# Optimization experiments

Hardware: AMD Instinct MI355X
Metric: run time of the kernel (lower is better)

Reference implementation:

```python
import jax, jax.numpy as jnp
import numpy as np

B, A, HR = 2, 180, 512
H_OUT = W_OUT = 512


def setup_inputs() -> dict:
    key = jax.random.key(0)
    k1, = jax.random.split(key, 1)
    sino = jax.random.normal(k1, (B, A, HR), dtype=jnp.float32)
    angles_deg = jnp.linspace(0.0, 180.0, A, endpoint=False, dtype=jnp.float32)
    return {"sino": sino, "angles_deg": angles_deg, "H": H_OUT, "W": W_OUT}


def _forward(sino, angles_deg, H, W):
    Bn, An, Hr = sino.shape
    pad = int(1.0 * 0.1 * min(H, W))  # pad_ratio = 1.0
    Hp, Wp = H + 2 * pad, W + 2 * pad

    # --- F.interpolate bilinear, align_corners=False: (A,B,Hr,1) -> (A,B,Hp,Wp).
    # Input width is 1, so width interp replicates the single column; only height interp matters.
    src = jnp.clip((jnp.arange(Hp, dtype=jnp.float32) + 0.5) * (Hr / Hp) - 0.5, 0.0, Hr - 1)
    i0 = jnp.floor(src).astype(jnp.int32)
    i1 = jnp.minimum(i0 + 1, Hr - 1)
    wH = src - i0.astype(jnp.float32)
    p = jnp.transpose(sino, (1, 0, 2)).astype(jnp.float32)  # (A,B,Hr)
    col = p[:, :, i0] * (1.0 - wH) + p[:, :, i1] * wH       # (A,B,Hp)
    proj = jnp.broadcast_to(col[:, :, :, None], (An, Bn, Hp, Wp))  # (A,B,Hp,Wp)

    # --- affine_grid (align_corners=False), sign = -1
    th = -jnp.deg2rad(angles_deg)
    c, s = jnp.cos(th), jnp.sin(th)                          # (A,)
    xs = (jnp.arange(Wp, dtype=jnp.float32) + 0.5) * (2.0 / Wp) - 1.0
    ys = (jnp.arange(Hp, dtype=jnp.float32) + 0.5) * (2.0 / Hp) - 1.0
    gx = c[:, None, None] * xs[None, None, :] - s[:, None, None] * ys[None, :, None]  # (A,Hp,Wp)
    gy = s[:, None, None] * xs[None, None, :] + c[:, None, None] * ys[None, :, None]

    # --- grid_sample bilinear, zeros padding, align_corners=False
    ix = ((gx + 1.0) * Wp - 1.0) * 0.5
    iy = ((gy + 1.0) * Hp - 1.0) * 0.5
    x0 = jnp.floor(ix).astype(jnp.int32); x1 = x0 + 1
    y0 = jnp.floor(iy).astype(jnp.int32); y1 = y0 + 1
    wx = ix - x0.astype(jnp.float32)
    wy = iy - y0.astype(jnp.float32)

    def corner(img, xi, yi, w):  # img (B,Hp,Wp); idx/w (Hp,Wp)
        valid = (xi >= 0) & (xi <= Wp - 1) & (yi >= 0) & (yi <= Hp - 1)
        xc = jnp.clip(xi, 0, Wp - 1)
        yc = jnp.clip(yi, 0, Hp - 1)
        return img[:, yc, xc] * (w * valid.astype(jnp.float32))[None]

    def sample(img, x0a, x1a, y0a, y1a, wxa, wya):
        return (corner(img, x0a, y0a, (1 - wxa) * (1 - wya)) +
                corner(img, x1a, y0a, wxa * (1 - wya)) +
                corner(img, x0a, y1a, (1 - wxa) * wya) +
                corner(img, x1a, y1a, wxa * wya))

    xr = jax.vmap(sample)(proj, x0, x1, y0, y1, wx, wy)      # (A,B,Hp,Wp)
    acc = xr.sum(axis=0) / (An + 1e-06)                      # (B,Hp,Wp)
    acc = acc[:, None, :, :]                                 # (B,1,Hp,Wp)
    if pad > 0:
        acc = acc[:, :, pad:Hp - pad, pad:Wp - pad]
    return acc


def reference(sino, angles_deg, H, W):
    return _forward(sino, angles_deg, H, W)
```

## Files before the change

### kernel.cpp

```cpp
#include <hip/hip_runtime.h>
#include <hip/hip_fp16.h>
#include <math.h>

#define B_N   2
#define A_N   180
#define HR_N  512
#define H_OUT 512
#define W_OUT 512
#define PAD   51
#define HP    614
#define WP    614
#define GUARD 80
#define HPP   (HP + 2*GUARD)
#define NPIX  (H_OUT * W_OUT)

#define TW    16
#define TH    8
#define QA    45
#define CH_Q  15
#define NCH   3
#define WIN   20


__device__ __forceinline__ float col_val(const float* __restrict__ sino,
                                         int b, int a, int yy) {
    if (yy < 0 || yy >= HP) return 0.0f;
    float src = ((float)yy + 0.5f) * ((float)HR_N / (float)HP) - 0.5f;
    src = fminf(fmaxf(src, 0.0f), (float)(HR_N - 1));
    int i0 = (int)floorf(src);
    int i1 = min(i0 + 1, HR_N - 1);
    float wH = src - (float)i0;
    const float* srow = sino + ((size_t)b * A_N + a) * HR_N;
    return srow[i0] * (1.0f - wH) + srow[i1] * wH;
}

__global__ void prep_kernel(const float* __restrict__ sino,
                            const float* __restrict__ angles,
                            uint2* __restrict__ pk2,
                            float2* __restrict__ tg) {
    int idx = blockIdx.x * blockDim.x + threadIdx.x;
    if (idx < A_N) {
        float th = -angles[idx] * (float)(M_PI / 180.0);
        tg[idx] = make_float2(cosf(th), sinf(th));
    }
    const int total = A_N * HPP;
    if (idx < total) {
        int y = idx % HPP;
        int a = idx / HPP;
        int yy = y - GUARD;
        float v00 = col_val(sino, 0, a, yy);
        float v10 = col_val(sino, 1, a, yy);
        float v01 = col_val(sino, 0, a, yy + 1);
        float v11 = col_val(sino, 1, a, yy + 1);
        __half2 lo = __floats2half2_rn(v00, v10);
        __half2 hi = __floats2half2_rn(v01, v11);
        uint2 u;
        u.x = *(unsigned int*)&lo;
        u.y = *(unsigned int*)&hi;
        pk2[idx] = u;
    }
}

template <bool INTERIOR>
__device__ __forceinline__ void bp_body(const uint2* __restrict__ pk2,
                                        const float4* __restrict__ s_cs,
                                        const unsigned* __restrict__ s_off,
                                        uint2* __restrict__ s_win,
                                        int t, int q, float X, float Y,
                                        float& a00, float& a01, float& a10, float& a11) {
    for (int ch = 0; ch < NCH; ++ch) {
        for (int e = t; e < 4 * CH_Q * WIN; e += 256) {
            int wid = e / WIN;
            int j   = e - wid * WIN;
            int qq  = wid / CH_Q;
            int la  = wid - qq * CH_Q;
            int a   = qq * QA + ch * CH_Q + la;
            s_win[e] = pk2[s_off[a] + (unsigned)j];
        }
        __syncthreads();

        const int abase = q * QA + ch * CH_Q;
        const int wbase = q * (CH_Q * WIN);
        if (INTERIOR) {
            __half2 h0 = __float2half2_rn(0.0f);
            __half2 h1 = __float2half2_rn(0.0f);
#pragma unroll
            for (int la = 0; la < CH_Q; ++la) {
                float4 cs = s_cs[abase + la];
                float c = cs.x, s = cs.y;
                float f0 = fmaf(s, X, fmaf(c, Y, cs.z));
                float f1 = f0 + s;
                int   li0 = (int)f0;  float wy0 = __builtin_amdgcn_fractf(f0);
                int   li1 = (int)f1;  float wy1 = f1 - (float)li1;
                uint2 cv0 = s_win[wbase + la * WIN + li0];
                uint2 cv1 = s_win[wbase + la * WIN + li1];
                __half2 lo0 = *(__half2*)&cv0.x, hi0 = *(__half2*)&cv0.y;
                __half2 lo1 = *(__half2*)&cv1.x, hi1 = *(__half2*)&cv1.y;
                h0 = __hadd2(h0, __hfma2(__float2half2_rn(wy0), __hsub2(hi0, lo0), lo0));
                h1 = __hadd2(h1, __hfma2(__float2half2_rn(wy1), __hsub2(hi1, lo1), lo1));
            }
            a00 += __low2float(h0);  a01 += __high2float(h0);
            a10 += __low2float(h1);  a11 += __high2float(h1);
        } else {
#pragma unroll
            for (int la = 0; la < CH_Q; ++la) {
                float4 cs = s_cs[abase + la];
                float c = cs.x, s = cs.y;
                float f0 = fmaf(s, X, fmaf(c, Y, cs.z));
                float f1 = f0 + s;
                int   li0 = (int)f0;  float wy0 = __builtin_amdgcn_fractf(f0);
                int   li1 = (int)f1;  float wy1 = f1 - (float)li1;
                uint2 cv0 = s_win[wbase + la * WIN + li0];
                uint2 cv1 = s_win[wbase + la * WIN + li1];
                __half2 lo0 = *(__half2*)&cv0.x, hi0 = *(__half2*)&cv0.y;
                __half2 lo1 = *(__half2*)&cv1.x, hi1 = *(__half2*)&cv1.y;
                __half2 r0 = __hfma2(__float2half2_rn(wy0), __hsub2(hi0, lo0), lo0);
                __half2 r1 = __hfma2(__float2half2_rn(wy1), __hsub2(hi1, lo1), lo1);
                float ix0 = fmaf(c, X, fmaf(-s, Y, 306.5f));
                float ix1 = ix0 + c;
                float xf0 = fminf(fmaxf(ix0 + 1.0f, 0.0f), 1.0f)
                          * fminf(fmaxf((float)WP - ix0, 0.0f), 1.0f);
                float xf1 = fminf(fmaxf(ix1 + 1.0f, 0.0f), 1.0f)
                          * fminf(fmaxf((float)WP - ix1, 0.0f), 1.0f);
                a00 = fmaf(xf0, __low2float(r0),  a00);
                a01 = fmaf(xf0, __high2float(r0), a01);
                a10 = fmaf(xf1, __low2float(r1),  a10);
                a11 = fmaf(xf1, __high2float(r1), a11);
            }
        }
        __syncthreads();
    }
}

__global__ __launch_bounds__(256, 8) void bp_kernel(const uint2* __restrict__ pk2,
                                                    const float2* __restrict__ tgv,
                                                    float* __restrict__ out) {
    __shared__ float4   s_cs[A_N];
    __shared__ unsigned s_off[A_N];
    __shared__ uint2    s_win[4 * CH_Q * WIN];
    __shared__ float    s_red[3][256];

    int t  = threadIdx.x;
    int tx = blockIdx.x, ty = blockIdx.y;
    float Xc = (float)(tx * TW) - 248.0f;
    float Yc = (float)(ty * TH) - 252.0f;

    if (t < A_N) {
        float2 cs = tgv[t];
        float iyc = fmaf(cs.y, Xc, fmaf(cs.x, Yc, 306.5f));
        int base = (int)floorf(iyc) - 9;
        s_cs[t]  = make_float4(cs.x, cs.y, 306.5f - (float)base, 0.0f);
        s_off[t] = (unsigned)(t * HPP + GUARD + base);
    }

    int q  = t >> 6;
    int tt = t & 63;
    int lx = (tt & 7) << 1;
    int ly = tt >> 3;
    float X = (float)(tx * TW + lx) - 255.5f;
    float Y = (float)(ty * TH + ly) - 255.5f;

    float a00 = 0.0f, a01 = 0.0f, a10 = 0.0f, a11 = 0.0f;
    __syncthreads();

    bool interior = (Xc * Xc + Yc * Yc) <= 87500.0f;
    if (interior)
        bp_body<true >(pk2, s_cs, s_off, s_win, t, q, X, Y, a00, a01, a10, a11);
    else
        bp_body<false>(pk2, s_cs, s_off, s_win, t, q, X, Y, a00, a01, a10, a11);

    int pix = ly * TW + lx;
    if (q != 0) {
        s_red[q - 1][pix]           = a00;
        s_red[q - 1][pix + 1]       = a10;
        s_red[q - 1][128 + pix]     = a01;
        s_red[q - 1][128 + pix + 1] = a11;
    }
    __syncthreads();
    if (q == 0) {
        const float inv = 1.0f / (180.0f + 1e-6f);
        float2 v0, v1;
        v0.x = (a00 + s_red[0][pix]       + s_red[1][pix]       + s_red[2][pix])       * inv;
        v0.y = (a10 + s_red[0][pix+1]     + s_red[1][pix+1]     + s_red[2][pix+1])     * inv;
        v1.x = (a01 + s_red[0][128+pix]   + s_red[1][128+pix]   + s_red[2][128+pix])   * inv;
        v1.y = (a11 + s_red[0][128+pix+1] + s_red[1][128+pix+1] + s_red[2][128+pix+1]) * inv;
        int idx = (ty * TH + ly) * W_OUT + (tx * TW + lx);
        *(float2*)(out + idx)        = v0;
        *(float2*)(out + NPIX + idx) = v1;
    }
}

extern "C" void kernel_launch(void* const* d_in, const int* in_sizes, int n_in,
                              void* d_out, int out_size, void* d_ws, size_t ws_size,
                              hipStream_t stream) {
    const float* sino   = (const float*)d_in[0];
    const float* angles = (const float*)d_in[1];
    char*   ws  = (char*)d_ws;
    uint2*  pk2 = (uint2*)ws;
    float2* tg  = (float2*)(ws + (size_t)A_N * HPP * sizeof(uint2));

    const int total = A_N * HPP;
    prep_kernel<<<(total + 255) / 256, 256, 0, stream>>>(sino, angles, pk2, tg);

    dim3 grid(W_OUT / TW, H_OUT / TH);
    bp_kernel<<<grid, 256, 0, stream>>>(pk2, tg, (float*)d_out);
}
```

Baseline: 82.34 us.

## Precompute per-tile angle tables in prep kernel and read them via scalar loads

The per-block setup that computed window bases and offsets for each angle moves into the prep kernel, which now writes a global table of (cos, sin, base offset, window offset) for every tile-angle pair. The back-projection loop reads that table from global memory, with readfirstlane marking the values as wave-uniform so the compiler can use scalar loads and drop the shared-memory copy. This removes the shared s_cs array and the per-block trig-derived setup. In exchange it adds a table of about 368K float4 entries written and read through global memory, and a larger prep grid.

```diff
diff --git a/kernel.cpp b/kernel.cpp
--- a/kernel.cpp
+++ b/kernel.cpp
@@ -21,6 +21,18 @@
 #define NCH   3
 #define WIN   20
 
+#define NTILE (32 * 64)
+#define PREP_BLKS  545
+#define TBL_BLKS   1440
+#define PK2_BYTES  ((size_t)A_N * HPP * sizeof(uint2))
+
+
+__device__ __forceinline__ float rf_f(float x) {
+    return __uint_as_float(__builtin_amdgcn_readfirstlane(__float_as_uint(x)));
+}
+__device__ __forceinline__ unsigned rf_u(unsigned x) {
+    return (unsigned)__builtin_amdgcn_readfirstlane((int)x);
+}
 
 __device__ __forceinline__ float col_val(const float* __restrict__ sino,
                                          int b, int a, int yy) {
@@ -37,33 +49,48 @@
 __global__ void prep_kernel(const float* __restrict__ sino,
                             const float* __restrict__ angles,
                             uint2* __restrict__ pk2,
-                            float2* __restrict__ tg) {
-    int idx = blockIdx.x * blockDim.x + threadIdx.x;
-    if (idx < A_N) {
-        float th = -angles[idx] * (float)(M_PI / 180.0);
-        tg[idx] = make_float2(cosf(th), sinf(th));
-    }
-    const int total = A_N * HPP;
-    if (idx < total) {
-        int y = idx % HPP;
-        int a = idx / HPP;
-        int yy = y - GUARD;
-        float v00 = col_val(sino, 0, a, yy);
-        float v10 = col_val(sino, 1, a, yy);
-        float v01 = col_val(sino, 0, a, yy + 1);
-        float v11 = col_val(sino, 1, a, yy + 1);
-        __half2 lo = __floats2half2_rn(v00, v10);
-        __half2 hi = __floats2half2_rn(v01, v11);
-        uint2 u;
-        u.x = *(unsigned int*)&lo;
-        u.y = *(unsigned int*)&hi;
-        pk2[idx] = u;
+                            float4* __restrict__ tbl) {
+    int bid = blockIdx.x;
+    int t   = threadIdx.x;
+    if (bid < PREP_BLKS) {
+        int idx = bid * 256 + t;
+        const int total = A_N * HPP;
+        if (idx < total) {
+            int y = idx % HPP;
+            int a = idx / HPP;
+            int yy = y - GUARD;
+            float v00 = col_val(sino, 0, a, yy);
+            float v10 = col_val(sino, 1, a, yy);
+            float v01 = col_val(sino, 0, a, yy + 1);
+            float v11 = col_val(sino, 1, a, yy + 1);
+            __half2 lo = __floats2half2_rn(v00, v10);
+            __half2 hi = __floats2half2_rn(v01, v11);
+            uint2 u;
+            u.x = *(unsigned int*)&lo;
+            u.y = *(unsigned int*)&hi;
+            pk2[idx] = u;
+        }
+    } else {
+        int e    = (bid - PREP_BLKS) * 256 + t;
+        unsigned tile = (unsigned)e / A_N;
+        int a    = e - (int)tile * A_N;
+        int tx   = (int)(tile & 31);
+        int ty   = (int)(tile >> 5);
+        float Xc = (float)(tx * TW) - 248.0f;
+        float Yc = (float)(ty * TH) - 252.0f;
+        float th = -angles[a] * (float)(M_PI / 180.0);
+        float c  = cosf(th);
+        float s  = sinf(th);
+        float iyc = fmaf(s, Xc, fmaf(c, Yc, 306.5f));
+        int base = (int)floorf(iyc) - 9;
+        tbl[e] = make_float4(c, s, 306.5f - (float)base,
+                             __uint_as_float((unsigned)(a * HPP + GUARD + base)));
     }
 }
 
 template <bool INTERIOR>
 __device__ __forceinline__ void bp_body(const uint2* __restrict__ pk2,
-                                        const float4* __restrict__ s_cs,
+                                        const float4* __restrict__ tb,
                                         const unsigned* __restrict__ s_off,
                                         uint2* __restrict__ s_win,
                                         int t, int q, float X, float Y,
@@ -79,16 +106,19 @@
         }
         __syncthreads();
 
-        const int abase = q * QA + ch * CH_Q;
+        const int abase = rf_u((unsigned)(q * QA + ch * CH_Q));
         const int wbase = q * (CH_Q * WIN);
         if (INTERIOR) {
             __half2 h0 = __float2half2_rn(0.0f);
             __half2 h1 = __float2half2_rn(0.0f);
 #pragma unroll
             for (int la = 0; la < CH_Q; ++la) {
-                float4 cs = s_cs[abase + la];
-                float c = cs.x, s = cs.y;
-                float f0 = fmaf(s, X, fmaf(c, Y, cs.z));
+                float4 ev = tb[abase + la];
+                float c  = rf_f(ev.x);
+                float s  = rf_f(ev.y);
+                float Kf = rf_f(ev.z);
+                unsigned off = rf_u(__float_as_uint(ev.w));
+                float f0 = fmaf(s, X, fmaf(c, Y, Kf));
                 float f1 = f0 + s;
                 int   li0 = (int)f0;  float wy0 = __builtin_amdgcn_fractf(f0);
                 int   li1 = (int)f1;  float wy1 = f1 - (float)li1;
@@ -104,9 +134,12 @@
         } else {
 #pragma unroll
             for (int la = 0; la < CH_Q; ++la) {
-                float4 cs = s_cs[abase + la];
-                float c = cs.x, s = cs.y;
-                float f0 = fmaf(s, X, fmaf(c, Y, cs.z));
+                float4 ev = tb[abase + la];
+                float c  = rf_f(ev.x);
+                float s  = rf_f(ev.y);
+                float Kf = rf_f(ev.z);
+                unsigned off = rf_u(__float_as_uint(ev.w));
+                float f0 = fmaf(s, X, fmaf(c, Y, Kf));
                 float f1 = f0 + s;
                 int   li0 = (int)f0;  float wy0 = __builtin_amdgcn_fractf(f0);
                 int   li1 = (int)f1;  float wy1 = f1 - (float)li1;
@@ -129,29 +162,23 @@
             }
         }
         __syncthreads();
+        (void)0;
     }
 }
 
 __global__ __launch_bounds__(256, 8) void bp_kernel(const uint2* __restrict__ pk2,
-                                                    const float2* __restrict__ tgv,
+                                                    const float4* __restrict__ tbl,
                                                     float* __restrict__ out) {
-    __shared__ float4   s_cs[A_N];
     __shared__ unsigned s_off[A_N];
     __shared__ uint2    s_win[4 * CH_Q * WIN];
     __shared__ float    s_red[3][256];
 
     int t  = threadIdx.x;
     int tx = blockIdx.x, ty = blockIdx.y;
-    float Xc = (float)(tx * TW) - 248.0f;
-    float Yc = (float)(ty * TH) - 252.0f;
-
-    if (t < A_N) {
-        float2 cs = tgv[t];
-        float iyc = fmaf(cs.y, Xc, fmaf(cs.x, Yc, 306.5f));
-        int base = (int)floorf(iyc) - 9;
-        s_cs[t]  = make_float4(cs.x, cs.y, 306.5f - (float)base, 0.0f);
-        s_off[t] = (unsigned)(t * HPP + GUARD + base);
-    }
+    unsigned tile = (unsigned)(ty * 32 + tx);
+    const float4* __restrict__ tb = tbl + (size_t)tile * A_N;
+
+    if (t < A_N) s_off[t] = __float_as_uint(tb[t].w);
 
     int q  = t >> 6;
     int tt = t & 63;
@@ -159,15 +186,17 @@
     int ly = tt >> 3;
     float X = (float)(tx * TW + lx) - 255.5f;
     float Y = (float)(ty * TH + ly) - 255.5f;
+    float Xc = (float)(tx * TW) - 248.0f;
+    float Yc = (float)(ty * TH) - 252.0f;
 
     float a00 = 0.0f, a01 = 0.0f, a10 = 0.0f, a11 = 0.0f;
     __syncthreads();
 
     bool interior = (Xc * Xc + Yc * Yc) <= 87500.0f;
     if (interior)
-        bp_body<true >(pk2, s_cs, s_off, s_win, t, q, X, Y, a00, a01, a10, a11);
+        bp_body<true >(pk2, tb, s_off, s_win, t, q, X, Y, a00, a01, a10, a11);
     else
-        bp_body<false>(pk2, s_cs, s_off, s_win, t, q, X, Y, a00, a01, a10, a11);
+        bp_body<false>(pk2, tb, s_off, s_win, t, q, X, Y, a00, a01, a10, a11);
 
     int pix = ly * TW + lx;
     if (q != 0) {
@@ -197,11 +226,10 @@
     const float* angles = (const float*)d_in[1];
     char*   ws  = (char*)d_ws;
     uint2*  pk2 = (uint2*)ws;
-    float2* tg  = (float2*)(ws + (size_t)A_N * HPP * sizeof(uint2));
-
-    const int total = A_N * HPP;
-    prep_kernel<<<(total + 255) / 256, 256, 0, stream>>>(sino, angles, pk2, tg);
+    float4* tbl = (float4*)(ws + PK2_BYTES);
+
+    prep_kernel<<<PREP_BLKS + TBL_BLKS, 256, 0, stream>>>(sino, angles, pk2, tbl);
 
     dim3 grid(W_OUT / TW, H_OUT / TH);
-    bp_kernel<<<grid, 256, 0, stream>>>(pk2, tg, (float*)d_out);
-}
+    bp_kernel<<<grid, 256, 0, stream>>>(pk2, tbl, (float*)d_out);
+}
```

After: 84.84 us. 1.03x slower.
